# Kernel tuning notes

Measured on AMD Instinct MI355X. Metric: run time of the kernel, lower is better.

## Reference

```python
import jax, jax.numpy as jnp
import numpy as np

N = 50000      # nodes
E = 800000     # edges
IN = 128       # in_dim
OUT = 64       # out_dim
NEG_SLOPE = 0.01  # F.leaky_relu default


def setup_inputs() -> dict:
    key = jax.random.key(0)
    k1, k2, k3, k4, k5 = jax.random.split(key, 5)
    h = jax.random.normal(k1, (N, IN), dtype=jnp.float32)
    # xavier-normal-ish scale for the two linear layers
    W_fc = jax.random.normal(k2, (OUT, IN), dtype=jnp.float32) * (2.0 / (IN + OUT)) ** 0.5
    W_attn = jax.random.normal(k3, (2 * OUT,), dtype=jnp.float32) * (2.0 / (2 * OUT + 1)) ** 0.5
    src = jax.random.randint(k4, (E,), 0, N)
    dst = jax.random.randint(k5, (E,), 0, N)
    return {"h": h, "W_fc": W_fc, "W_attn": W_attn, "src": src, "dst": dst}


def reference(h, W_fc, W_attn, src, dst):
    # z = fc(h): [N, OUT]
    z = jnp.einsum("ni,oi->no", h, W_fc)
    d = z.shape[-1]
    # per-edge attention logit: attn_fc(cat([z_src, z_dst])) == z_src@a_l + z_dst@a_r
    a_l, a_r = W_attn[:d], W_attn[d:]
    zs = z[src]                                   # [E, OUT] gather
    e = jax.nn.leaky_relu(zs @ a_l + z[dst] @ a_r, negative_slope=NEG_SLOPE)  # [E]
    # segment softmax over incoming edges of each dst node
    m = jax.ops.segment_max(e, dst, num_segments=N)          # [N]
    ex = jnp.exp(e - m[dst])                                  # [E]
    denom = jax.ops.segment_sum(ex, dst, num_segments=N)      # [N]
    alpha = ex / denom[dst]                                    # [E]
    # weighted scatter-sum of source features
    out = jax.ops.segment_sum(alpha[:, None] * zs, dst, num_segments=N)  # [N, OUT]
    return out
```

## Files before the change

kernel.cpp:

```cpp
#include <hip/hip_runtime.h>
#include <hip/hip_bf16.h>
#include <math.h>

#define IN_DIM 128
#define OUT_DIM 64
#define NEG_SLOPE 0.01f
#define BCAP 8192
#define EPT 16

typedef __attribute__((ext_vector_type(8))) short bf8_t;
typedef __attribute__((ext_vector_type(4))) float f4_t;

__device__ __forceinline__ bf8_t pack8(float4 a, float4 b) {
    union { bf8_t v; __hip_bfloat162 h[4]; } u;
    u.h[0] = __float22bfloat162_rn(make_float2(a.x, a.y));
    u.h[1] = __float22bfloat162_rn(make_float2(a.z, a.w));
    u.h[2] = __float22bfloat162_rn(make_float2(b.x, b.y));
    u.h[3] = __float22bfloat162_rn(make_float2(b.z, b.w));
    return u.v;
}

__global__ __launch_bounds__(256) void k_part1(
    const int* __restrict__ src, const int* __restrict__ dst,
    int* __restrict__ bucket_cursor, unsigned* __restrict__ tmp,
    int E, int NB)
{
    __shared__ int cnt[256];
    __shared__ int cur[256];
    const int t = threadIdx.x;
    const int base_e = blockIdx.x * (256 * EPT);

    cnt[t] = 0;
    __syncthreads();

    unsigned pArr[EPT];
    #pragma unroll
    for (int i = 0; i < EPT; i++) {
        int ei = base_e + i * 256 + t;
        if (ei < E) {
            int s = src[ei], d = dst[ei];
            int b = d >> 8;
            pArr[i] = ((unsigned)b << 24) | ((unsigned)s << 8) | (unsigned)(d & 255);
            atomicAdd(&cnt[b], 1);
        } else {
            pArr[i] = 0xFFFFFFFFu;
        }
    }
    __syncthreads();

    if (t < NB && cnt[t] > 0)
        cur[t] = atomicAdd(&bucket_cursor[t], cnt[t]);
    __syncthreads();

    #pragma unroll
    for (int i = 0; i < EPT; i++) {
        unsigned p = pArr[i];
        if (p == 0xFFFFFFFFu) continue;
        int b = p >> 24;
        int slot = atomicAdd(&cur[b], 1);
        tmp[(size_t)b * BCAP + slot] = p;
    }
}

__global__ __launch_bounds__(256) void k_mid(
    const unsigned* __restrict__ tmp, const int* __restrict__ bucket_cnt,
    unsigned short* __restrict__ edge_src, int* __restrict__ offsets,
    int* __restrict__ counts,
    const float4* __restrict__ h4, const float4* __restrict__ W4,
    const float* __restrict__ Wattn,
    __hip_bfloat16* __restrict__ zb, float* __restrict__ s_l, float* __restrict__ s_r,
    int N, int NB)
{
    __shared__ int sh[256];
    __shared__ int cnt[256];
    __shared__ int cur[256];

    if (blockIdx.x < NB) {
        const int b = blockIdx.x, t = threadIdx.x;

        int v = (t < NB) ? bucket_cnt[t] : 0;
        sh[t] = v;
        __syncthreads();
        for (int o = 1; o < 256; o <<= 1) {
            int x = (t >= o) ? sh[t - o] : 0;
            __syncthreads();
            sh[t] += x;
            __syncthreads();
        }
        const int mb   = bucket_cnt[b];
        const int base = sh[b] - mb;
        __syncthreads();

        cnt[t] = 0;
        __syncthreads();

        const unsigned* mybuf = tmp + (size_t)b * BCAP;
        for (int i = t; i < mb; i += 256)
            atomicAdd(&cnt[mybuf[i] & 255u], 1);
        __syncthreads();

        int c = cnt[t];
        sh[t] = c;
        __syncthreads();
        for (int o = 1; o < 256; o <<= 1) {
            int x = (t >= o) ? sh[t - o] : 0;
            __syncthreads();
            sh[t] += x;
            __syncthreads();
        }
        cur[t] = sh[t] - c;
        const int node = b * 256 + t;
        if (node < N) {
            counts[node]  = c;
            offsets[node] = base + (sh[t] - c);
        }
        __syncthreads();

        for (int i = t; i < mb; i += 256) {
            unsigned p = mybuf[i];
            int d = p & 255u;
            int s = (p >> 8) & 0xFFFFu;
            int slot = atomicAdd(&cur[d], 1);
            edge_src[base + slot] = (unsigned short)s;
        }
    } else {
        const int lane = threadIdx.x & 63;
        const int wv   = threadIdx.x >> 6;
        const int col  = lane & 15, quad = lane >> 4;
        const int n0   = (blockIdx.x - NB) * 64 + wv * 16;
        if (n0 >= N) return;

        bf8_t bf[4][4];
        #pragma unroll
        for (int ns = 0; ns < 4; ns++) {
            const float4* wrow = W4 + (size_t)(ns * 16 + col) * (IN_DIM / 4);
            #pragma unroll
            for (int kb = 0; kb < 4; kb++) {
                float4 x = wrow[kb * 8 + quad * 2];
                float4 y = wrow[kb * 8 + quad * 2 + 1];
                bf[kb][ns] = pack8(x, y);
            }
        }

        const int  na = n0 + col;
        const bool nv = (na < N);
        const float4* hrow = h4 + (size_t)(nv ? na : 0) * (IN_DIM / 4);
        const float4 zero = make_float4(0.f, 0.f, 0.f, 0.f);

        f4_t acc[4];
        #pragma unroll
        for (int ns = 0; ns < 4; ns++) acc[ns] = (f4_t){0.f, 0.f, 0.f, 0.f};

        #pragma unroll
        for (int kb = 0; kb < 4; kb++) {
            float4 x = nv ? hrow[kb * 8 + quad * 2]     : zero;
            float4 y = nv ? hrow[kb * 8 + quad * 2 + 1] : zero;
            bf8_t a = pack8(x, y);
            #pragma unroll
            for (int ns = 0; ns < 4; ns++)
                acc[ns] = __builtin_amdgcn_mfma_f32_16x16x32_bf16(a, bf[kb][ns], acc[ns], 0, 0, 0);
        }

        float alv[4], arv[4];
        #pragma unroll
        for (int ns = 0; ns < 4; ns++) {
            alv[ns] = Wattn[ns * 16 + col];
            arv[ns] = Wattn[OUT_DIM + ns * 16 + col];
        }
        #pragma unroll
        for (int r = 0; r < 4; r++) {
            const int nn = n0 + quad * 4 + r;
            float pl = acc[0][r] * alv[0] + acc[1][r] * alv[1] + acc[2][r] * alv[2] + acc[3][r] * alv[3];
            float pr = acc[0][r] * arv[0] + acc[1][r] * arv[1] + acc[2][r] * arv[2] + acc[3][r] * arv[3];
            #pragma unroll
            for (int o = 1; o < 16; o <<= 1) {
                pl += __shfl_xor(pl, o, 64);
                pr += __shfl_xor(pr, o, 64);
            }
            if (nn < N) {
                __hip_bfloat16* zr = zb + (size_t)nn * OUT_DIM;
                #pragma unroll
                for (int ns = 0; ns < 4; ns++)
                    zr[ns * 16 + col] = __float2bfloat16(acc[ns][r]);
                if (col == 0) { s_l[nn] = pl; s_r[nn] = pr; }
            }
        }
    }
}

__global__ __launch_bounds__(256) void k_node(
    const int* __restrict__ offsets, const int* __restrict__ counts,
    const unsigned short* __restrict__ edge_src,
    const float* __restrict__ s_l, const float* __restrict__ s_r,
    const uint2* __restrict__ zb2, float4* __restrict__ out4, int N)
{
    const int lane = threadIdx.x & 63;
    const int node = blockIdx.x * 4 + (threadIdx.x >> 6);
    if (node >= N) return;

    const int beg = offsets[node];
    const int deg = counts[node];
    const int end = beg + deg;
    const int c4 = lane & 15;
    const int g  = lane >> 4;

    if (deg == 0) {
        if (lane < 16) out4[(size_t)node * 16 + lane] = make_float4(0.f, 0.f, 0.f, 0.f);
        return;
    }

    const float sr = s_r[node];
    float4 acc = make_float4(0.f, 0.f, 0.f, 0.f);
    float dsum = 0.f;

    for (int cs = beg; cs < end; cs += 64) {
        int i = cs + lane;
        int s_my = 0; float ex_my = 0.f;
        if (i < end) {
            s_my = edge_src[i];
            float e = s_l[s_my] + sr;
            e = (e > 0.f) ? e : NEG_SLOPE * e;
            ex_my = __expf(e);
        }
        dsum += ex_my;
        int cnt = end - cs; if (cnt > 64) cnt = 64;
        for (int j = 0; j < cnt; j += 4) {
            int jj = j + g;
            int   s  = __shfl(s_my, jj & 63, 64);
            float ex = __shfl(ex_my, jj & 63, 64);
            if (jj >= cnt) ex = 0.f;
            union { uint2 u; __hip_bfloat162 h[2]; } zu;
            zu.u = zb2[(size_t)s * 16 + c4];
            float2 f0 = __bfloat1622float2(zu.h[0]);
            float2 f1 = __bfloat1622float2(zu.h[1]);
            acc.x += ex * f0.x; acc.y += ex * f0.y;
            acc.z += ex * f1.x; acc.w += ex * f1.y;
        }
    }

    #pragma unroll
    for (int off = 16; off <= 32; off <<= 1) {
        acc.x += __shfl_xor(acc.x, off, 64);
        acc.y += __shfl_xor(acc.y, off, 64);
        acc.z += __shfl_xor(acc.z, off, 64);
        acc.w += __shfl_xor(acc.w, off, 64);
    }
    #pragma unroll
    for (int off = 32; off; off >>= 1) dsum += __shfl_xor(dsum, off, 64);

    if (lane < 16) {
        float inv = 1.f / dsum;
        out4[(size_t)node * 16 + c4] =
            make_float4(acc.x * inv, acc.y * inv, acc.z * inv, acc.w * inv);
    }
}

extern "C" void kernel_launch(void* const* d_in, const int* in_sizes, int n_in,
                              void* d_out, int out_size, void* d_ws, size_t ws_size,
                              hipStream_t stream)
{
    const float* h     = (const float*)d_in[0];
    const float* Wfc   = (const float*)d_in[1];
    const float* Wattn = (const float*)d_in[2];
    const int*   src   = (const int*)d_in[3];
    const int*   dst   = (const int*)d_in[4];
    const int N = in_sizes[0] / IN_DIM;
    const int E = in_sizes[3];
    const int NB = (N + 255) / 256;

    __hip_bfloat16* zb = (__hip_bfloat16*)d_ws;
    float* s_l      = (float*)(zb + (size_t)N * OUT_DIM);
    float* s_r      = s_l + N;
    int*   counts   = (int*)(s_r + N);
    int*   offsets  = counts + N;
    int*   bcursor  = offsets + N;
    unsigned short* edge_src = (unsigned short*)(bcursor + 256);
    size_t esz = ((size_t)E + 1) & ~(size_t)1;
    unsigned* tmp = (unsigned*)(edge_src + esz);

    const int nblk_g = (N + 63) / 64;
    const int nblk1  = (E + 256 * EPT - 1) / (256 * EPT);

    hipMemsetAsync(bcursor, 0, 256 * sizeof(int), stream);

    k_part1<<<nblk1, 256, 0, stream>>>(src, dst, bcursor, tmp, E, NB);
    k_mid  <<<NB + nblk_g, 256, 0, stream>>>(tmp, bcursor, edge_src, offsets, counts,
                                             (const float4*)h, (const float4*)Wfc, Wattn,
                                             zb, s_l, s_r, N, NB);
    k_node <<<(N + 3) / 4, 256, 0, stream>>>(offsets, counts, edge_src, s_l, s_r,
                                             (const uint2*)zb, (float4*)d_out, N);
}
```

Measured before the change: 153.6 us.

## Replace CSR build with bucketed shared-memory accumulation and fuse partition with GEMM

Drops the per-node CSR sort kernel. Edges are partitioned into 128-node buckets in the same launch as the fc GEMM. A per-bucket kernel then accumulates exp-weighted source features and denominators with LDS atomics before normalizing. This removes one launch and the edge_src/offsets round trip through global memory. In exchange, every edge-feature product goes through an LDS atomic add, and bucket capacity is halved.

```diff
diff --git a/kernel.cpp b/kernel.cpp
--- a/kernel.cpp
+++ b/kernel.cpp
@@ -5,7 +5,7 @@
 #define IN_DIM 128
 #define OUT_DIM 64
 #define NEG_SLOPE 0.01f
-#define BCAP 8192
+#define BCAP 4096
 #define EPT 16
 
 typedef __attribute__((ext_vector_type(8))) short bf8_t;
@@ -20,114 +20,57 @@
     return u.v;
 }
 
-__global__ __launch_bounds__(256) void k_part1(
+__global__ __launch_bounds__(256) void k_front(
     const int* __restrict__ src, const int* __restrict__ dst,
-    int* __restrict__ bucket_cursor, unsigned* __restrict__ tmp,
-    int E, int NB)
-{
-    __shared__ int cnt[256];
-    __shared__ int cur[256];
-    const int t = threadIdx.x;
-    const int base_e = blockIdx.x * (256 * EPT);
-
-    cnt[t] = 0;
-    __syncthreads();
-
-    unsigned pArr[EPT];
-    #pragma unroll
-    for (int i = 0; i < EPT; i++) {
-        int ei = base_e + i * 256 + t;
-        if (ei < E) {
-            int s = src[ei], d = dst[ei];
-            int b = d >> 8;
-            pArr[i] = ((unsigned)b << 24) | ((unsigned)s << 8) | (unsigned)(d & 255);
-            atomicAdd(&cnt[b], 1);
-        } else {
-            pArr[i] = 0xFFFFFFFFu;
-        }
-    }
-    __syncthreads();
-
-    if (t < NB && cnt[t] > 0)
-        cur[t] = atomicAdd(&bucket_cursor[t], cnt[t]);
-    __syncthreads();
-
-    #pragma unroll
-    for (int i = 0; i < EPT; i++) {
-        unsigned p = pArr[i];
-        if (p == 0xFFFFFFFFu) continue;
-        int b = p >> 24;
-        int slot = atomicAdd(&cur[b], 1);
-        tmp[(size_t)b * BCAP + slot] = p;
-    }
-}
-
-__global__ __launch_bounds__(256) void k_mid(
-    const unsigned* __restrict__ tmp, const int* __restrict__ bucket_cnt,
-    unsigned short* __restrict__ edge_src, int* __restrict__ offsets,
-    int* __restrict__ counts,
+    int* __restrict__ bucket_cursor, unsigned* __restrict__ tmp, int E,
     const float4* __restrict__ h4, const float4* __restrict__ W4,
     const float* __restrict__ Wattn,
     __hip_bfloat16* __restrict__ zb, float* __restrict__ s_l, float* __restrict__ s_r,
-    int N, int NB)
+    int N, int NP1)
 {
-    __shared__ int sh[256];
-    __shared__ int cnt[256];
-    __shared__ int cur[256];
-
-    if (blockIdx.x < NB) {
-        const int b = blockIdx.x, t = threadIdx.x;
-
-        int v = (t < NB) ? bucket_cnt[t] : 0;
-        sh[t] = v;
+    __shared__ int cnt[512];
+    __shared__ int cur[512];
+
+    if (blockIdx.x < NP1) {
+        const int t = threadIdx.x;
+        const int base_e = blockIdx.x * (256 * EPT);
+
+        cnt[t] = 0; cnt[t + 256] = 0;
         __syncthreads();
-        for (int o = 1; o < 256; o <<= 1) {
-            int x = (t >= o) ? sh[t - o] : 0;
-            __syncthreads();
-            sh[t] += x;
-            __syncthreads();
-        }
-        const int mb   = bucket_cnt[b];
-        const int base = sh[b] - mb;
+
+        unsigned pArr[EPT];
+        #pragma unroll
+        for (int i = 0; i < EPT; i++) {
+            int ei = base_e + i * 256 + t;
+            if (ei < E) {
+                int s = src[ei], d = dst[ei];
+                int b = d >> 7;
+                pArr[i] = ((unsigned)b << 23) | ((unsigned)s << 7) | (unsigned)(d & 127);
+                atomicAdd(&cnt[b], 1);
+            } else {
+                pArr[i] = 0xFFFFFFFFu;
+            }
+        }
         __syncthreads();
 
-        cnt[t] = 0;
+        for (int b = t; b < 512; b += 256)
+            if (cnt[b] > 0)
+                cur[b] = atomicAdd(&bucket_cursor[b], cnt[b]);
         __syncthreads();
 
-        const unsigned* mybuf = tmp + (size_t)b * BCAP;
-        for (int i = t; i < mb; i += 256)
-            atomicAdd(&cnt[mybuf[i] & 255u], 1);
-        __syncthreads();
-
-        int c = cnt[t];
-        sh[t] = c;
-        __syncthreads();
-        for (int o = 1; o < 256; o <<= 1) {
-            int x = (t >= o) ? sh[t - o] : 0;
-            __syncthreads();
-            sh[t] += x;
-            __syncthreads();
-        }
-        cur[t] = sh[t] - c;
-        const int node = b * 256 + t;
-        if (node < N) {
-            counts[node]  = c;
-            offsets[node] = base + (sh[t] - c);
-        }
-        __syncthreads();
-
-        for (int i = t; i < mb; i += 256) {
-            unsigned p = mybuf[i];
-            int d = p & 255u;
-            int s = (p >> 8) & 0xFFFFu;
-            int slot = atomicAdd(&cur[d], 1);
-            edge_src[base + slot] = (unsigned short)s;
+        #pragma unroll
+        for (int i = 0; i < EPT; i++) {
+            unsigned p = pArr[i];
+            if (p == 0xFFFFFFFFu) continue;
+            int b = p >> 23;
+            int slot = atomicAdd(&cur[b], 1);
+            tmp[(size_t)b * BCAP + slot] = p;
         }
     } else {
         const int lane = threadIdx.x & 63;
         const int wv   = threadIdx.x >> 6;
         const int col  = lane & 15, quad = lane >> 4;
-        const int n0   = (blockIdx.x - NB) * 64 + wv * 16;
+        const int n0   = (blockIdx.x - NP1) * 64 + wv * 16;
         if (n0 >= N) return;
 
         bf8_t bf[4][4];
@@ -188,70 +131,66 @@
     }
 }
 
-__global__ __launch_bounds__(256) void k_node(
-    const int* __restrict__ offsets, const int* __restrict__ counts,
-    const unsigned short* __restrict__ edge_src,
+__global__ __launch_bounds__(512) void k_bucket(
+    const unsigned* __restrict__ tmp, const int* __restrict__ bucket_cnt,
     const float* __restrict__ s_l, const float* __restrict__ s_r,
-    const uint2* __restrict__ zb2, float4* __restrict__ out4, int N)
+    const unsigned short* __restrict__ zb16,
+    float4* __restrict__ out4, int N)
 {
-    const int lane = threadIdx.x & 63;
-    const int node = blockIdx.x * 4 + (threadIdx.x >> 6);
-    if (node >= N) return;
-
-    const int beg = offsets[node];
-    const int deg = counts[node];
-    const int end = beg + deg;
-    const int c4 = lane & 15;
-    const int g  = lane >> 4;
-
-    if (deg == 0) {
-        if (lane < 16) out4[(size_t)node * 16 + lane] = make_float4(0.f, 0.f, 0.f, 0.f);
-        return;
-    }
-
-    const float sr = s_r[node];
-    float4 acc = make_float4(0.f, 0.f, 0.f, 0.f);
-    float dsum = 0.f;
-
-    for (int cs = beg; cs < end; cs += 64) {
-        int i = cs + lane;
-        int s_my = 0; float ex_my = 0.f;
-        if (i < end) {
-            s_my = edge_src[i];
-            float e = s_l[s_my] + sr;
+    __shared__ float acc_s[128 * 64];
+    __shared__ float den_s[128];
+    __shared__ float srs[128];
+
+    const int b = blockIdx.x, t = threadIdx.x;
+    const int lane = t & 63, wv = t >> 6;
+    const int mb = bucket_cnt[b];
+    const int nbase = b * 128;
+
+    for (int i = t; i < 128 * 16; i += 512)
+        ((float4*)acc_s)[i] = make_float4(0.f, 0.f, 0.f, 0.f);
+    if (t < 128) {
+        int n = nbase + t;
+        den_s[t] = 0.f;
+        srs[t] = (n < N) ? s_r[n] : 0.f;
+    }
+    __syncthreads();
+
+    const unsigned* mybuf = tmp + (size_t)b * BCAP;
+    for (int base = wv * 64; base < mb; base += 512) {
+        int i = base + lane;
+        bool valid = (i < mb);
+        unsigned p = valid ? mybuf[i] : 0u;
+        int s_my = (p >> 7) & 0xFFFFu;
+        float ex_my = 0.f;
+        if (valid) {
+            int dlow = p & 127u;
+            float e = s_l[s_my] + srs[dlow];
             e = (e > 0.f) ? e : NEG_SLOPE * e;
             ex_my = __expf(e);
-        }
-        dsum += ex_my;
-        int cnt = end - cs; if (cnt > 64) cnt = 64;
-        for (int j = 0; j < cnt; j += 4) {
-            int jj = j + g;
-            int   s  = __shfl(s_my, jj & 63, 64);
-            float ex = __shfl(ex_my, jj & 63, 64);
-            if (jj >= cnt) ex = 0.f;
-            union { uint2 u; __hip_bfloat162 h[2]; } zu;
-            zu.u = zb2[(size_t)s * 16 + c4];
-            float2 f0 = __bfloat1622float2(zu.h[0]);
-            float2 f1 = __bfloat1622float2(zu.h[1]);
-            acc.x += ex * f0.x; acc.y += ex * f0.y;
-            acc.z += ex * f1.x; acc.w += ex * f1.y;
-        }
-    }
-
-    #pragma unroll
-    for (int off = 16; off <= 32; off <<= 1) {
-        acc.x += __shfl_xor(acc.x, off, 64);
-        acc.y += __shfl_xor(acc.y, off, 64);
-        acc.z += __shfl_xor(acc.z, off, 64);
-        acc.w += __shfl_xor(acc.w, off, 64);
-    }
-    #pragma unroll
-    for (int off = 32; off; off >>= 1) dsum += __shfl_xor(dsum, off, 64);
-
-    if (lane < 16) {
-        float inv = 1.f / dsum;
-        out4[(size_t)node * 16 + c4] =
-            make_float4(acc.x * inv, acc.y * inv, acc.z * inv, acc.w * inv);
+            atomicAdd(&den_s[dlow], ex_my);
+        }
+        int cnt = mb - base; if (cnt > 64) cnt = 64;
+        for (int j = 0; j < cnt; ++j) {
+            unsigned pj = __shfl(p, j, 64);
+            float ex = __shfl(ex_my, j, 64);
+            int d = pj & 127u;
+            int s = (pj >> 7) & 0xFFFFu;
+            float zv = __uint_as_float((unsigned)zb16[(size_t)s * 64 + lane] << 16);
+            atomicAdd(&acc_s[d * 64 + lane], ex * zv);
+        }
+    }
+    __syncthreads();
+
+    for (int i = t; i < 128 * 16; i += 512) {
+        int nl = i >> 4;
+        int n = nbase + nl;
+        if (n < N) {
+            float den = den_s[nl];
+            float inv = (den > 0.f) ? 1.f / den : 0.f;
+            float4 v = ((float4*)acc_s)[i];
+            out4[(size_t)n * 16 + (i & 15)] =
+                make_float4(v.x * inv, v.y * inv, v.z * inv, v.w * inv);
+        }
     }
 }
 
@@ -266,27 +205,22 @@
     const int*   dst   = (const int*)d_in[4];
     const int N = in_sizes[0] / IN_DIM;
     const int E = in_sizes[3];
-    const int NB = (N + 255) / 256;
+    const int NBK = (N + 127) / 128;
+    const int NP1 = (E + 256 * EPT - 1) / (256 * EPT);
 
     __hip_bfloat16* zb = (__hip_bfloat16*)d_ws;
-    float* s_l      = (float*)(zb + (size_t)N * OUT_DIM);
-    float* s_r      = s_l + N;
-    int*   counts   = (int*)(s_r + N);
-    int*   offsets  = counts + N;
-    int*   bcursor  = offsets + N;
-    unsigned short* edge_src = (unsigned short*)(bcursor + 256);
-    size_t esz = ((size_t)E + 1) & ~(size_t)1;
-    unsigned* tmp = (unsigned*)(edge_src + esz);
+    float* s_l     = (float*)(zb + (size_t)N * OUT_DIM);
+    float* s_r     = s_l + N;
+    int*   bcursor = (int*)(s_r + N);
+    unsigned* tmp  = (unsigned*)(bcursor + 512);
 
     const int nblk_g = (N + 63) / 64;
-    const int nblk1  = (E + 256 * EPT - 1) / (256 * EPT);
-
-    hipMemsetAsync(bcursor, 0, 256 * sizeof(int), stream);
-
-    k_part1<<<nblk1, 256, 0, stream>>>(src, dst, bcursor, tmp, E, NB);
-    k_mid  <<<NB + nblk_g, 256, 0, stream>>>(tmp, bcursor, edge_src, offsets, counts,
-                                             (const float4*)h, (const float4*)Wfc, Wattn,
-                                             zb, s_l, s_r, N, NB);
-    k_node <<<(N + 3) / 4, 256, 0, stream>>>(offsets, counts, edge_src, s_l, s_r,
-                                             (const uint2*)zb, (float4*)d_out, N);
-}
+
+    hipMemsetAsync(bcursor, 0, 512 * sizeof(int), stream);
+
+    k_front <<<NP1 + nblk_g, 256, 0, stream>>>(src, dst, bcursor, tmp, E,
+                                               (const float4*)h, (const float4*)Wfc, Wattn,
+                                               zb, s_l, s_r, N, NP1);
+    k_bucket<<<NBK, 512, 0, stream>>>(tmp, bcursor, s_l, s_r,
+                                      (const unsigned short*)zb, (float4*)d_out, N);
+}
```

Result: slower. 495.2 us (+222.4%).
